# Optimization experiments

Measured on AMD Instinct MI355X. Metric: run time of the kernel, lower is better.

Reference implementation:

```python
import jax, jax.numpy as jnp
import numpy as np

HEAD_SIZE = 64
EMB_SIZE = 1024
B, N = 4, 4096


def setup_inputs() -> dict:
    key = jax.random.key(0)
    kx, kk, kq, kv = jax.random.split(key, 4)
    x = jax.random.normal(kx, (B, N, EMB_SIZE), dtype=jnp.float32)
    # nn.Linear(emb, head, bias=False): weight [head, emb]; y = x @ W.T
    s = 1.0 / np.sqrt(EMB_SIZE)
    Wk = jax.random.uniform(kk, (HEAD_SIZE, EMB_SIZE), jnp.float32, -s, s)
    Wq = jax.random.uniform(kq, (HEAD_SIZE, EMB_SIZE), jnp.float32, -s, s)
    Wv = jax.random.uniform(kv, (HEAD_SIZE, EMB_SIZE), jnp.float32, -s, s)
    return {"x": x, "Wk": Wk, "Wq": Wq, "Wv": Wv}


def reference(x, Wk, Wq, Wv):
    # k, q, v: [B, N, H]
    k = jnp.einsum("bne,he->bnh", x, Wk)
    q = jnp.einsum("bne,he->bnh", x, Wq)
    v = jnp.einsum("bne,he->bnh", x, Wv)
    scale = HEAD_SIZE ** -0.5
    aff = jnp.einsum("bqh,bkh->bqk", q, k) * scale  # [B, N, N]
    aff = jax.nn.softmax(aff, axis=2)
    # dropout rate is 0.0 -> identity
    return jnp.einsum("bqk,bkh->bqh", aff, v)
```

## Files before the change

### kernel.cpp

```cpp
#include <hip/hip_runtime.h>

#define NB   4
#define SEQ  4096
#define EMB  1024
#define HS   64

typedef __attribute__((ext_vector_type(8))) short bf16x8;
typedef __attribute__((ext_vector_type(4))) float f32x4;

__device__ inline unsigned short f2bf(float f) {
  unsigned int u = __float_as_uint(f);
  u += 0x7fffu + ((u >> 16) & 1u);
  return (unsigned short)(u >> 16);
}
__device__ inline float bf2f(unsigned short h) {
  return __uint_as_float(((unsigned int)h) << 16);
}
__device__ inline int swzi64(int row, int c) {
  return row * 64 + ((c ^ (row & 7)) << 3);
}
__device__ inline int swzi32(int row, int c) {
  return row * 32 + ((c ^ ((row >> 1) & 3)) << 3);
}
__device__ inline int swzi128(int row, int c) {
  return row * 128 + ((c ^ (row & 7)) << 3);
}
__device__ inline void gld16(const unsigned short* g, unsigned short* l) {
  __builtin_amdgcn_global_load_lds(
      (const __attribute__((address_space(1))) void*)g,
      (__attribute__((address_space(3))) void*)l, 16, 0, 0);
}

__global__ __launch_bounds__(256) void wprep(
    const float* __restrict__ Wk, const float* __restrict__ Wq,
    const float* __restrict__ Wv,
    unsigned short* __restrict__ Wh, unsigned short* __restrict__ Wl) {
  int i = blockIdx.x * 256 + threadIdx.x;
  int e = i >> 8, c = i & 255;
  float4 v;
  float sc = 1.0f;
  if (e < 64)       { v = ((const float4*)Wq)[e * 256 + c];
                      sc = 0.18033688011112042f; }
  else if (e < 128)   v = ((const float4*)Wk)[(e - 64) * 256 + c];
  else                v = ((const float4*)Wv)[(e - 128) * 256 + c];
  v.x *= sc; v.y *= sc; v.z *= sc; v.w *= sc;
  ushort4 hv, lv;
  hv.x = f2bf(v.x); lv.x = f2bf(v.x - bf2f(hv.x));
  hv.y = f2bf(v.y); lv.y = f2bf(v.y - bf2f(hv.y));
  hv.z = f2bf(v.z); lv.z = f2bf(v.z - bf2f(hv.z));
  hv.w = f2bf(v.w); lv.w = f2bf(v.w - bf2f(hv.w));
  *(ushort4*)&Wh[i * 4] = hv;
  *(ushort4*)&Wl[i * 4] = lv;
}

#define XhSp(p) ((unsigned short*)(SM + (p) * 2048))
#define XlSp(p) ((unsigned short*)(SM + 4096 + (p) * 2048))
#define WhSp(p) ((unsigned short*)(SM + 8192 + (p) * 12288))
#define WlSp(p) ((unsigned short*)(SM + 32768 + (p) * 12288))

__global__ __launch_bounds__(256) void qkv_x1(
    const float* __restrict__ x,
    const unsigned short* __restrict__ Wh, const unsigned short* __restrict__ Wl,
    unsigned short* __restrict__ qh, unsigned short* __restrict__ ql,
    unsigned short* __restrict__ kh, unsigned short* __restrict__ kl,
    unsigned short* __restrict__ vt) {
  __shared__ __align__(16) unsigned char SM[57344];

  const int t  = threadIdx.x;
  const int l  = t & 63;
  const int li = l & 15;
  const int g  = l >> 4;
  const int w  = t >> 6;
  const int m0 = blockIdx.x * 32;
  const int b  = m0 >> 12;
  const int n0 = m0 & 4095;

  const int xrow = t >> 3;
  const float* xp = x + (m0 + xrow) * EMB + (t & 7) * 4;
  const int xaddr = xrow * 32 + ((((t & 7) >> 1) ^ ((xrow >> 1) & 3)) << 3)
                    + (t & 1) * 4;

  const int wconst = (l >> 2) * EMB + (((l & 3) ^ ((l >> 3) & 3)) << 3);

  f32x4 acc[2][3];
#pragma unroll
  for (int i = 0; i < 2; ++i)
#pragma unroll
    for (int j = 0; j < 3; ++j) acc[i][j] = (f32x4){0.f, 0.f, 0.f, 0.f};

  const int rA0 = li, rA1 = 16 + li;
  const int rB0 = 48 * w + li, rB1 = rB0 + 16, rB2 = rB0 + 32;

  auto issueW = [&](int s, int p) {
    const int ko = s * 32;
#pragma unroll
    for (int i = 0; i < 3; ++i) {
      const int seg = 3 * w + i;
      gld16(Wh + 16 * seg * EMB + wconst + ko, WhSp(p) + seg * 512);
      gld16(Wl + 16 * seg * EMB + wconst + ko, WlSp(p) + seg * 512);
    }
  };
  auto writeX = [&](float4 v, int p) {
    unsigned short h0 = f2bf(v.x), h1 = f2bf(v.y), h2 = f2bf(v.z), h3 = f2bf(v.w);
    unsigned short e0 = f2bf(v.x - bf2f(h0)), e1 = f2bf(v.y - bf2f(h1));
    unsigned short e2 = f2bf(v.z - bf2f(h2)), e3 = f2bf(v.w - bf2f(h3));
    int2 hv, lv;
    hv.x = (int)((unsigned)h0 | ((unsigned)h1 << 16));
    hv.y = (int)((unsigned)h2 | ((unsigned)h3 << 16));
    lv.x = (int)((unsigned)e0 | ((unsigned)e1 << 16));
    lv.y = (int)((unsigned)e2 | ((unsigned)e3 << 16));
    *(int2*)&XhSp(p)[xaddr] = hv;
    *(int2*)&XlSp(p)[xaddr] = lv;
  };

  float4 px = *(const float4*)xp;
  issueW(0, 0);
  writeX(px, 0);
  px = *(const float4*)(xp + 32);
  __syncthreads();

  for (int s = 0; s < 32; ++s) {
    const int p = s & 1;
    if (s < 31) {
      issueW(s + 1, p ^ 1);
      writeX(px, p ^ 1);
      if (s < 30) px = *(const float4*)(xp + (s + 2) * 32);
    } else {
      asm volatile("s_waitcnt vmcnt(0)" ::: "memory");
    }
    __builtin_amdgcn_sched_barrier(0);

    bf16x8 ah0 = *(const bf16x8*)&XhSp(p)[swzi32(rA0, g)];
    bf16x8 ah1 = *(const bf16x8*)&XhSp(p)[swzi32(rA1, g)];
    bf16x8 al0 = *(const bf16x8*)&XlSp(p)[swzi32(rA0, g)];
    bf16x8 al1 = *(const bf16x8*)&XlSp(p)[swzi32(rA1, g)];
    bf16x8 bh0 = *(const bf16x8*)&WhSp(p)[swzi32(rB0, g)];
    bf16x8 bh1 = *(const bf16x8*)&WhSp(p)[swzi32(rB1, g)];
    bf16x8 bh2 = *(const bf16x8*)&WhSp(p)[swzi32(rB2, g)];
    bf16x8 bl0 = *(const bf16x8*)&WlSp(p)[swzi32(rB0, g)];
    bf16x8 bl1 = *(const bf16x8*)&WlSp(p)[swzi32(rB1, g)];
    bf16x8 bl2 = *(const bf16x8*)&WlSp(p)[swzi32(rB2, g)];

    __builtin_amdgcn_s_setprio(1);
    acc[0][0] = __builtin_amdgcn_mfma_f32_16x16x32_bf16(ah0, bh0, acc[0][0], 0,0,0);
    acc[0][0] = __builtin_amdgcn_mfma_f32_16x16x32_bf16(ah0, bl0, acc[0][0], 0,0,0);
    acc[0][0] = __builtin_amdgcn_mfma_f32_16x16x32_bf16(al0, bh0, acc[0][0], 0,0,0);
    acc[0][1] = __builtin_amdgcn_mfma_f32_16x16x32_bf16(ah0, bh1, acc[0][1], 0,0,0);
    acc[0][1] = __builtin_amdgcn_mfma_f32_16x16x32_bf16(ah0, bl1, acc[0][1], 0,0,0);
    acc[0][1] = __builtin_amdgcn_mfma_f32_16x16x32_bf16(al0, bh1, acc[0][1], 0,0,0);
    acc[0][2] = __builtin_amdgcn_mfma_f32_16x16x32_bf16(ah0, bh2, acc[0][2], 0,0,0);
    acc[0][2] = __builtin_amdgcn_mfma_f32_16x16x32_bf16(ah0, bl2, acc[0][2], 0,0,0);
    acc[0][2] = __builtin_amdgcn_mfma_f32_16x16x32_bf16(al0, bh2, acc[0][2], 0,0,0);
    acc[1][0] = __builtin_amdgcn_mfma_f32_16x16x32_bf16(ah1, bh0, acc[1][0], 0,0,0);
    acc[1][0] = __builtin_amdgcn_mfma_f32_16x16x32_bf16(ah1, bl0, acc[1][0], 0,0,0);
    acc[1][0] = __builtin_amdgcn_mfma_f32_16x16x32_bf16(al1, bh0, acc[1][0], 0,0,0);
    acc[1][1] = __builtin_amdgcn_mfma_f32_16x16x32_bf16(ah1, bh1, acc[1][1], 0,0,0);
    acc[1][1] = __builtin_amdgcn_mfma_f32_16x16x32_bf16(ah1, bl1, acc[1][1], 0,0,0);
    acc[1][1] = __builtin_amdgcn_mfma_f32_16x16x32_bf16(al1, bh1, acc[1][1], 0,0,0);
    acc[1][2] = __builtin_amdgcn_mfma_f32_16x16x32_bf16(ah1, bh2, acc[1][2], 0,0,0);
    acc[1][2] = __builtin_amdgcn_mfma_f32_16x16x32_bf16(ah1, bl2, acc[1][2], 0,0,0);
    acc[1][2] = __builtin_amdgcn_mfma_f32_16x16x32_bf16(al1, bh2, acc[1][2], 0,0,0);
    __builtin_amdgcn_s_setprio(0);

    asm volatile("s_waitcnt lgkmcnt(0)" ::: "memory");
    __builtin_amdgcn_s_barrier();
    __builtin_amdgcn_sched_barrier(0);
  }

#pragma unroll
  for (int i = 0; i < 2; ++i)
#pragma unroll
    for (int j = 0; j < 3; ++j) {
      const int H3 = 48 * w + 16 * j + li;
#pragma unroll
      for (int r = 0; r < 4; ++r) {
        const int mrow = 16 * i + 4 * g + r;
        const float vv = acc[i][j][r];
        if (H3 < 64) {
          const unsigned short hb = f2bf(vv);
          const int off = (b * SEQ + n0 + mrow) * HS + H3;
          qh[off] = hb; ql[off] = f2bf(vv - bf2f(hb));
        } else if (H3 < 128) {
          const unsigned short hb = f2bf(vv);
          const int off = (b * SEQ + n0 + mrow) * HS + (H3 - 64);
          kh[off] = hb; kl[off] = f2bf(vv - bf2f(hb));
        } else {
          vt[(b * HS + (H3 - 128)) * SEQ + n0 + mrow] = f2bf(vv);
        }
      }
    }
}

__global__ __launch_bounds__(512) void attn_mfma(
    const unsigned short* __restrict__ qh, const unsigned short* __restrict__ ql,
    const unsigned short* __restrict__ kh, const unsigned short* __restrict__ kl,
    const unsigned short* __restrict__ vt, float* __restrict__ out) {
  __shared__ __align__(16) unsigned char SM[118784];
  unsigned short* const PtS = (unsigned short*)(SM + 98304);

  const int t  = threadIdx.x;
  const int l  = t & 63;
  const int li = l & 15;
  const int g  = l >> 4;
  const int w  = t >> 6;
  const int qg = w & 1;
  const int ks = w >> 1;
  const int b  = blockIdx.y;
  const int q0 = blockIdx.x << 6;

  bf16x8 qfh[2][2], qfl[2][2];
#pragma unroll
  for (int qs = 0; qs < 2; ++qs) {
    const unsigned short* qrh = qh + (b * SEQ + q0 + 32 * qg + 16 * qs + li) * HS;
    const unsigned short* qrl = ql + (b * SEQ + q0 + 32 * qg + 16 * qs + li) * HS;
    qfh[qs][0] = *(const bf16x8*)&qrh[8 * g];
    qfh[qs][1] = *(const bf16x8*)&qrh[32 + 8 * g];
    qfl[qs][0] = *(const bf16x8*)&qrl[8 * g];
    qfl[qs][1] = *(const bf16x8*)&qrl[32 + 8 * g];
  }

  const int kconst = (l >> 3) * HS + (((l & 7) ^ (l >> 3)) << 3);
  const int rowl = l >> 4, slot = l & 15;
  const int vcE = rowl * SEQ + ((slot ^ rowl) << 3);
  const int vcO = rowl * SEQ + ((slot ^ (4 + rowl)) << 3);
  const unsigned short* khB = kh + b * SEQ * HS;
  const unsigned short* klB = kl + b * SEQ * HS;
  const unsigned short* vtB = vt + b * HS * SEQ;
  const int sA = 2 * w, sB = 2 * w + 1;

  f32x4 O[4][2];
#pragma unroll
  for (int ht = 0; ht < 4; ++ht) {
    O[ht][0] = (f32x4){0.f, 0.f, 0.f, 0.f};
    O[ht][1] = (f32x4){0.f, 0.f, 0.f, 0.f};
  }
  float lp0 = 0.f, lp1 = 0.f;
  unsigned short* const PtW = PtS + w * 1280;

  auto stage = [&](int it, int p) {
    const int kt0 = it << 7;
    unsigned short* const KhP = (unsigned short*)(SM + p * 16384);
    unsigned short* const KlP = (unsigned short*)(SM + 32768 + p * 16384);
    unsigned short* const VtP = (unsigned short*)(SM + 65536 + p * 16384);
    gld16(khB + (kt0 + 8 * sA) * HS + kconst, KhP + sA * 512);
    gld16(khB + (kt0 + 8 * sB) * HS + kconst, KhP + sB * 512);
    gld16(klB + (kt0 + 8 * sA) * HS + kconst, KlP + sA * 512);
    gld16(klB + (kt0 + 8 * sB) * HS + kconst, KlP + sB * 512);
    gld16(vtB + 4 * sA * SEQ + kt0 + vcE, VtP + sA * 512);
    gld16(vtB + 4 * sB * SEQ + kt0 + vcO, VtP + sB * 512);
  };

  stage(0, 0);
  __syncthreads();

  for (int it = 0; it < 32; ++it) {
    const int p = it & 1;
    if (it < 31) stage(it + 1, p ^ 1);

    unsigned short* const KhS = (unsigned short*)(SM + p * 16384);
    unsigned short* const KlS = (unsigned short*)(SM + 32768 + p * 16384);
    unsigned short* const VtS = (unsigned short*)(SM + 65536 + p * 16384);

    f32x4 S[2][2];
    S[0][0] = (f32x4){-32.f, -32.f, -32.f, -32.f};
    S[0][1] = (f32x4){-32.f, -32.f, -32.f, -32.f};
    S[1][0] = (f32x4){-32.f, -32.f, -32.f, -32.f};
    S[1][1] = (f32x4){-32.f, -32.f, -32.f, -32.f};
    __builtin_amdgcn_s_setprio(1);
#pragma unroll
    for (int khf = 0; khf < 2; ++khf) {
      const int cc = 4 * khf + g;
#pragma unroll
      for (int kt = 0; kt < 2; ++kt) {
        const int row = 32 * ks + 16 * kt + li;
        bf16x8 akh = *(const bf16x8*)&KhS[swzi64(row, cc)];
        bf16x8 akl = *(const bf16x8*)&KlS[swzi64(row, cc)];
        S[kt][0] = __builtin_amdgcn_mfma_f32_16x16x32_bf16(akh, qfh[0][khf], S[kt][0], 0,0,0);
        S[kt][0] = __builtin_amdgcn_mfma_f32_16x16x32_bf16(akh, qfl[0][khf], S[kt][0], 0,0,0);
        S[kt][0] = __builtin_amdgcn_mfma_f32_16x16x32_bf16(akl, qfh[0][khf], S[kt][0], 0,0,0);
        S[kt][1] = __builtin_amdgcn_mfma_f32_16x16x32_bf16(akh, qfh[1][khf], S[kt][1], 0,0,0);
        S[kt][1] = __builtin_amdgcn_mfma_f32_16x16x32_bf16(akh, qfl[1][khf], S[kt][1], 0,0,0);
        S[kt][1] = __builtin_amdgcn_mfma_f32_16x16x32_bf16(akl, qfh[1][khf], S[kt][1], 0,0,0);
      }
    }
    __builtin_amdgcn_s_setprio(0);

#pragma unroll
    for (int kt = 0; kt < 2; ++kt)
#pragma unroll
      for (int qs = 0; qs < 2; ++qs) {
        unsigned pu[4];
        float ls = 0.f;
#pragma unroll
        for (int r = 0; r < 4; ++r) {
          const float pe = exp2f(S[kt][qs][r]);
          pu[r] = __float_as_uint(pe);
          ls += __uint_as_float(pu[r] & 0xffff0000u);
        }
        if (qs == 0) lp0 += ls; else lp1 += ls;
        const unsigned p01 = __builtin_amdgcn_perm(pu[1], pu[0], 0x07060302u);
        const unsigned p23 = __builtin_amdgcn_perm(pu[3], pu[2], 0x07060302u);
        const int qrow = 16 * qs + li;
        const int c = 2 * kt + (g >> 1);
        const int addr = qrow * 40 + (((c ^ (qrow & 3))) << 3) + ((g & 1) << 2);
        int2 pv; pv.x = (int)p01; pv.y = (int)p23;
        *(int2*)&PtW[addr] = pv;
      }

    asm volatile("" ::: "memory");

    bf16x8 pb0 = *(const bf16x8*)&PtW[li * 40 + ((g ^ (li & 3)) << 3)];
    {
      const int r1 = 16 + li;
      bf16x8 pb1 = *(const bf16x8*)&PtW[r1 * 40 + ((g ^ (r1 & 3)) << 3)];
      __builtin_amdgcn_s_setprio(1);
#pragma unroll
      for (int ht = 0; ht < 4; ++ht) {
        const int vrow = 16 * ht + li;
        bf16x8 va = *(const bf16x8*)&VtS[swzi128(vrow, 4 * ks + g)];
        O[ht][0] = __builtin_amdgcn_mfma_f32_16x16x32_bf16(va, pb0, O[ht][0], 0,0,0);
        O[ht][1] = __builtin_amdgcn_mfma_f32_16x16x32_bf16(va, pb1, O[ht][1], 0,0,0);
      }
      __builtin_amdgcn_s_setprio(0);
    }

    __syncthreads();
  }


  lp0 += __shfl_xor(lp0, 16); lp0 += __shfl_xor(lp0, 32);
  lp1 += __shfl_xor(lp1, 16); lp1 += __shfl_xor(lp1, 32);

  float* const OTm = (float*)SM;
  float* const Lm  = (float*)(SM + 65536);
#pragma unroll
  for (int ht = 0; ht < 4; ++ht)
#pragma unroll
    for (int qs = 0; qs < 2; ++qs) {
      float4 o4;
      o4.x = O[ht][qs][0]; o4.y = O[ht][qs][1];
      o4.z = O[ht][qs][2]; o4.w = O[ht][qs][3];
      *(float4*)&OTm[w * 2048 + (16 * qs + li) * 64 + 16 * ht + 4 * g] = o4;
    }
  if (g == 0) { Lm[w * 32 + li] = lp0; Lm[w * 32 + 16 + li] = lp1; }
  __syncthreads();

  {
    const int q = t >> 3, h8 = (t & 7) << 3;
    const int qq = q & 31, qgf = q >> 5;
    float lF = 0.f;
    float4 a = {0.f, 0.f, 0.f, 0.f}, c4 = {0.f, 0.f, 0.f, 0.f};
#pragma unroll
    for (int k2 = 0; k2 < 4; ++k2) {
      const int ww = qgf + 2 * k2;
      lF += Lm[ww * 32 + qq];
      const float* Ob = OTm + ww * 2048 + qq * 64 + h8;
      float4 u = *(const float4*)Ob;
      float4 v = *(const float4*)(Ob + 4);
      a.x += u.x; a.y += u.y; a.z += u.z; a.w += u.w;
      c4.x += v.x; c4.y += v.y; c4.z += v.z; c4.w += v.w;
    }
    const float inv = 1.f / lF;
    a.x *= inv; a.y *= inv; a.z *= inv; a.w *= inv;
    c4.x *= inv; c4.y *= inv; c4.z *= inv; c4.w *= inv;
    float* op = out + (b * SEQ + q0 + q) * HS + h8;
    *(float4*)op = a;
    *(float4*)(op + 4) = c4;
  }
}

extern "C" void kernel_launch(void* const* d_in, const int* in_sizes, int n_in,
                              void* d_out, int out_size, void* d_ws,
                              size_t ws_size, hipStream_t stream) {
  const float* x  = (const float*)d_in[0];
  const float* Wk = (const float*)d_in[1];
  const float* Wq = (const float*)d_in[2];
  const float* Wv = (const float*)d_in[3];
  float* out = (float*)d_out;

  unsigned short* us = (unsigned short*)d_ws;
  unsigned short* qh = us + 0 * (1 << 20);
  unsigned short* ql = us + 1 * (1 << 20);
  unsigned short* kh = us + 2 * (1 << 20);
  unsigned short* kl = us + 3 * (1 << 20);
  unsigned short* vt = us + 4 * (1 << 20);
  unsigned short* Wh = us + 5 * (1 << 20);
  unsigned short* Wl = Wh + 192 * 1024;

  wprep<<<192, 256, 0, stream>>>(Wk, Wq, Wv, Wh, Wl);
  qkv_x1<<<512, 256, 0, stream>>>(x, Wh, Wl, qh, ql, kh, kl, vt);
  attn_mfma<<<dim3(64, NB), 512, 0, stream>>>(qh, ql, kh, kl, vt, out);
}
```

Baseline: 186.8 us.

## Load QKV weight fragments directly into registers instead of staging through LDS

The QKV projection kernel now reads the bf16 hi/lo weight fragments straight from global memory into double-buffered registers, dropping the 48KB LDS staging buffers for weights. Shared memory falls to 8KB, and launch bounds request two blocks per CU to raise occupancy. The x prefetch is deepened to two steps ahead, and the LDS write is moved after the MFMAs. The risk is that each wave re-reads weights from L2/global with less coalesced 16-byte loads, and register pressure rises.

```diff
diff --git a/kernel.cpp b/kernel.cpp
--- a/kernel.cpp
+++ b/kernel.cpp
@@ -55,16 +55,14 @@
 
 #define XhSp(p) ((unsigned short*)(SM + (p) * 2048))
 #define XlSp(p) ((unsigned short*)(SM + 4096 + (p) * 2048))
-#define WhSp(p) ((unsigned short*)(SM + 8192 + (p) * 12288))
-#define WlSp(p) ((unsigned short*)(SM + 32768 + (p) * 12288))
-
-__global__ __launch_bounds__(256) void qkv_x1(
+
+__global__ __launch_bounds__(256, 2) void qkv_x1(
     const float* __restrict__ x,
     const unsigned short* __restrict__ Wh, const unsigned short* __restrict__ Wl,
     unsigned short* __restrict__ qh, unsigned short* __restrict__ ql,
     unsigned short* __restrict__ kh, unsigned short* __restrict__ kl,
     unsigned short* __restrict__ vt) {
-  __shared__ __align__(16) unsigned char SM[57344];
+  __shared__ __align__(16) unsigned char SM[8192];
 
   const int t  = threadIdx.x;
   const int l  = t & 63;
@@ -80,7 +78,13 @@
   const int xaddr = xrow * 32 + ((((t & 7) >> 1) ^ ((xrow >> 1) & 3)) << 3)
                     + (t & 1) * 4;
 
-  const int wconst = (l >> 2) * EMB + (((l & 3) ^ ((l >> 3) & 3)) << 3);
+  const int r0 = 48 * w + li, r1 = r0 + 16, r2 = r0 + 32;
+  const unsigned short* const Wh0 = Wh + r0 * EMB + 8 * g;
+  const unsigned short* const Wh1 = Wh + r1 * EMB + 8 * g;
+  const unsigned short* const Wh2 = Wh + r2 * EMB + 8 * g;
+  const unsigned short* const Wl0 = Wl + r0 * EMB + 8 * g;
+  const unsigned short* const Wl1 = Wl + r1 * EMB + 8 * g;
+  const unsigned short* const Wl2 = Wl + r2 * EMB + 8 * g;
 
   f32x4 acc[2][3];
 #pragma unroll
@@ -89,16 +93,15 @@
     for (int j = 0; j < 3; ++j) acc[i][j] = (f32x4){0.f, 0.f, 0.f, 0.f};
 
   const int rA0 = li, rA1 = 16 + li;
-  const int rB0 = 48 * w + li, rB1 = rB0 + 16, rB2 = rB0 + 32;
-
-  auto issueW = [&](int s, int p) {
+
+  auto loadB = [&](int s, bf16x8 (&B)[6]) {
     const int ko = s * 32;
-#pragma unroll
-    for (int i = 0; i < 3; ++i) {
-      const int seg = 3 * w + i;
-      gld16(Wh + 16 * seg * EMB + wconst + ko, WhSp(p) + seg * 512);
-      gld16(Wl + 16 * seg * EMB + wconst + ko, WlSp(p) + seg * 512);
-    }
+    B[0] = *(const bf16x8*)&Wh0[ko];
+    B[1] = *(const bf16x8*)&Wh1[ko];
+    B[2] = *(const bf16x8*)&Wh2[ko];
+    B[3] = *(const bf16x8*)&Wl0[ko];
+    B[4] = *(const bf16x8*)&Wl1[ko];
+    B[5] = *(const bf16x8*)&Wl2[ko];
   };
   auto writeX = [&](float4 v, int p) {
     unsigned short h0 = f2bf(v.x), h1 = f2bf(v.y), h2 = f2bf(v.z), h3 = f2bf(v.w);
@@ -113,58 +116,57 @@
     *(int2*)&XlSp(p)[xaddr] = lv;
   };
 
-  float4 px = *(const float4*)xp;
-  issueW(0, 0);
-  writeX(px, 0);
-  px = *(const float4*)(xp + 32);
+  bf16x8 B0[6], B1[6];
+  loadB(0, B0);
+  writeX(*(const float4*)xp, 0);
+  float4 pxA = *(const float4*)(xp + 32);
+  float4 pxB = *(const float4*)(xp + 64);
   __syncthreads();
 
-  for (int s = 0; s < 32; ++s) {
+  auto step = [&](int s, bf16x8 (&Bc)[6], bf16x8 (&Bn)[6]) {
     const int p = s & 1;
-    if (s < 31) {
-      issueW(s + 1, p ^ 1);
-      writeX(px, p ^ 1);
-      if (s < 30) px = *(const float4*)(xp + (s + 2) * 32);
-    } else {
-      asm volatile("s_waitcnt vmcnt(0)" ::: "memory");
-    }
-    __builtin_amdgcn_sched_barrier(0);
+    if (s < 31) loadB(s + 1, Bn);
 
     bf16x8 ah0 = *(const bf16x8*)&XhSp(p)[swzi32(rA0, g)];
     bf16x8 ah1 = *(const bf16x8*)&XhSp(p)[swzi32(rA1, g)];
     bf16x8 al0 = *(const bf16x8*)&XlSp(p)[swzi32(rA0, g)];
     bf16x8 al1 = *(const bf16x8*)&XlSp(p)[swzi32(rA1, g)];
-    bf16x8 bh0 = *(const bf16x8*)&WhSp(p)[swzi32(rB0, g)];
-    bf16x8 bh1 = *(const bf16x8*)&WhSp(p)[swzi32(rB1, g)];
-    bf16x8 bh2 = *(const bf16x8*)&WhSp(p)[swzi32(rB2, g)];
-    bf16x8 bl0 = *(const bf16x8*)&WlSp(p)[swzi32(rB0, g)];
-    bf16x8 bl1 = *(const bf16x8*)&WlSp(p)[swzi32(rB1, g)];
-    bf16x8 bl2 = *(const bf16x8*)&WlSp(p)[swzi32(rB2, g)];
 
     __builtin_amdgcn_s_setprio(1);
-    acc[0][0] = __builtin_amdgcn_mfma_f32_16x16x32_bf16(ah0, bh0, acc[0][0], 0,0,0);
-    acc[0][0] = __builtin_amdgcn_mfma_f32_16x16x32_bf16(ah0, bl0, acc[0][0], 0,0,0);
-    acc[0][0] = __builtin_amdgcn_mfma_f32_16x16x32_bf16(al0, bh0, acc[0][0], 0,0,0);
-    acc[0][1] = __builtin_amdgcn_mfma_f32_16x16x32_bf16(ah0, bh1, acc[0][1], 0,0,0);
-    acc[0][1] = __builtin_amdgcn_mfma_f32_16x16x32_bf16(ah0, bl1, acc[0][1], 0,0,0);
-    acc[0][1] = __builtin_amdgcn_mfma_f32_16x16x32_bf16(al0, bh1, acc[0][1], 0,0,0);
-    acc[0][2] = __builtin_amdgcn_mfma_f32_16x16x32_bf16(ah0, bh2, acc[0][2], 0,0,0);
-    acc[0][2] = __builtin_amdgcn_mfma_f32_16x16x32_bf16(ah0, bl2, acc[0][2], 0,0,0);
-    acc[0][2] = __builtin_amdgcn_mfma_f32_16x16x32_bf16(al0, bh2, acc[0][2], 0,0,0);
-    acc[1][0] = __builtin_amdgcn_mfma_f32_16x16x32_bf16(ah1, bh0, acc[1][0], 0,0,0);
-    acc[1][0] = __builtin_amdgcn_mfma_f32_16x16x32_bf16(ah1, bl0, acc[1][0], 0,0,0);
-    acc[1][0] = __builtin_amdgcn_mfma_f32_16x16x32_bf16(al1, bh0, acc[1][0], 0,0,0);
-    acc[1][1] = __builtin_amdgcn_mfma_f32_16x16x32_bf16(ah1, bh1, acc[1][1], 0,0,0);
-    acc[1][1] = __builtin_amdgcn_mfma_f32_16x16x32_bf16(ah1, bl1, acc[1][1], 0,0,0);
-    acc[1][1] = __builtin_amdgcn_mfma_f32_16x16x32_bf16(al1, bh1, acc[1][1], 0,0,0);
-    acc[1][2] = __builtin_amdgcn_mfma_f32_16x16x32_bf16(ah1, bh2, acc[1][2], 0,0,0);
-    acc[1][2] = __builtin_amdgcn_mfma_f32_16x16x32_bf16(ah1, bl2, acc[1][2], 0,0,0);
-    acc[1][2] = __builtin_amdgcn_mfma_f32_16x16x32_bf16(al1, bh2, acc[1][2], 0,0,0);
+    acc[0][0] = __builtin_amdgcn_mfma_f32_16x16x32_bf16(ah0, Bc[0], acc[0][0], 0,0,0);
+    acc[0][0] = __builtin_amdgcn_mfma_f32_16x16x32_bf16(ah0, Bc[3], acc[0][0], 0,0,0);
+    acc[0][0] = __builtin_amdgcn_mfma_f32_16x16x32_bf16(al0, Bc[0], acc[0][0], 0,0,0);
+    acc[0][1] = __builtin_amdgcn_mfma_f32_16x16x32_bf16(ah0, Bc[1], acc[0][1], 0,0,0);
+    acc[0][1] = __builtin_amdgcn_mfma_f32_16x16x32_bf16(ah0, Bc[4], acc[0][1], 0,0,0);
+    acc[0][1] = __builtin_amdgcn_mfma_f32_16x16x32_bf16(al0, Bc[1], acc[0][1], 0,0,0);
+    acc[0][2] = __builtin_amdgcn_mfma_f32_16x16x32_bf16(ah0, Bc[2], acc[0][2], 0,0,0);
+    acc[0][2] = __builtin_amdgcn_mfma_f32_16x16x32_bf16(ah0, Bc[5], acc[0][2], 0,0,0);
+    acc[0][2] = __builtin_amdgcn_mfma_f32_16x16x32_bf16(al0, Bc[2], acc[0][2], 0,0,0);
+    acc[1][0] = __builtin_amdgcn_mfma_f32_16x16x32_bf16(ah1, Bc[0], acc[1][0], 0,0,0);
+    acc[1][0] = __builtin_amdgcn_mfma_f32_16x16x32_bf16(ah1, Bc[3], acc[1][0], 0,0,0);
+    acc[1][0] = __builtin_amdgcn_mfma_f32_16x16x32_bf16(al1, Bc[0], acc[1][0], 0,0,0);
+    acc[1][1] = __builtin_amdgcn_mfma_f32_16x16x32_bf16(ah1, Bc[1], acc[1][1], 0,0,0);
+    acc[1][1] = __builtin_amdgcn_mfma_f32_16x16x32_bf16(ah1, Bc[4], acc[1][1], 0,0,0);
+    acc[1][1] = __builtin_amdgcn_mfma_f32_16x16x32_bf16(al1, Bc[1], acc[1][1], 0,0,0);
+    acc[1][2] = __builtin_amdgcn_mfma_f32_16x16x32_bf16(ah1, Bc[2], acc[1][2], 0,0,0);
+    acc[1][2] = __builtin_amdgcn_mfma_f32_16x16x32_bf16(ah1, Bc[5], acc[1][2], 0,0,0);
+    acc[1][2] = __builtin_amdgcn_mfma_f32_16x16x32_bf16(al1, Bc[2], acc[1][2], 0,0,0);
     __builtin_amdgcn_s_setprio(0);
+
+    if (s < 31) {
+      writeX(pxA, p ^ 1);
+      pxA = pxB;
+      if (s < 29) pxB = *(const float4*)(xp + (s + 3) * 32);
+    }
 
     asm volatile("s_waitcnt lgkmcnt(0)" ::: "memory");
     __builtin_amdgcn_s_barrier();
     __builtin_amdgcn_sched_barrier(0);
+  };
+
+  for (int s2 = 0; s2 < 16; ++s2) {
+    step(2 * s2,     B0, B1);
+    step(2 * s2 + 1, B1, B0);
   }
 
 #pragma unroll
```

Measured after the change: 197.8 us. +5.9%, slower.

## Software-pipeline PV matmul one iteration behind QK and exp

Applied to the files above, without the earlier changes.

Splits each attention iteration so the P·V MFMA for the previous key tile runs right after the current QK^T MFMAs, while the exp/pack of the current tile follows. V gets a triple-buffered LDS slot and P gets a double-buffered per-wave slab, which raises shared memory from about 116KB to 152KB. The aim is to interleave the exp work with the matrix-core work and to drop the in-iteration dependency between writing P and reading it back. The cost is more LDS, an extra epilogue PV call, and added register pressure.

```diff
diff --git a/kernel.cpp b/kernel.cpp
--- a/kernel.cpp
+++ b/kernel.cpp
@@ -195,8 +195,8 @@
     const unsigned short* __restrict__ qh, const unsigned short* __restrict__ ql,
     const unsigned short* __restrict__ kh, const unsigned short* __restrict__ kl,
     const unsigned short* __restrict__ vt, float* __restrict__ out) {
-  __shared__ __align__(16) unsigned char SM[118784];
-  unsigned short* const PtS = (unsigned short*)(SM + 98304);
+  __shared__ __align__(16) unsigned char SM[155648];
+  unsigned short* const PtS = (unsigned short*)(SM + 114688);
 
   const int t  = threadIdx.x;
   const int l  = t & 63;
@@ -235,13 +235,12 @@
     O[ht][1] = (f32x4){0.f, 0.f, 0.f, 0.f};
   }
   float lp0 = 0.f, lp1 = 0.f;
-  unsigned short* const PtW = PtS + w * 1280;
-
-  auto stage = [&](int it, int p) {
+
+  auto stage = [&](int it, int pK, int vb) {
     const int kt0 = it << 7;
-    unsigned short* const KhP = (unsigned short*)(SM + p * 16384);
-    unsigned short* const KlP = (unsigned short*)(SM + 32768 + p * 16384);
-    unsigned short* const VtP = (unsigned short*)(SM + 65536 + p * 16384);
+    unsigned short* const KhP = (unsigned short*)(SM + pK * 16384);
+    unsigned short* const KlP = (unsigned short*)(SM + 32768 + pK * 16384);
+    unsigned short* const VtP = (unsigned short*)(SM + 65536 + vb * 16384);
     gld16(khB + (kt0 + 8 * sA) * HS + kconst, KhP + sA * 512);
     gld16(khB + (kt0 + 8 * sB) * HS + kconst, KhP + sB * 512);
     gld16(klB + (kt0 + 8 * sA) * HS + kconst, KlP + sA * 512);
@@ -250,16 +249,34 @@
     gld16(vtB + 4 * sB * SEQ + kt0 + vcO, VtP + sB * 512);
   };
 
-  stage(0, 0);
+  auto PV = [&](int slab, int vb) {
+    unsigned short* const PtP = PtS + w * 2560 + slab * 1280;
+    unsigned short* const VtP = (unsigned short*)(SM + 65536 + vb * 16384);
+    bf16x8 pb0 = *(const bf16x8*)&PtP[li * 40 + ((g ^ (li & 3)) << 3)];
+    const int r1 = 16 + li;
+    bf16x8 pb1 = *(const bf16x8*)&PtP[r1 * 40 + ((g ^ (r1 & 3)) << 3)];
+    __builtin_amdgcn_s_setprio(1);
+#pragma unroll
+    for (int ht = 0; ht < 4; ++ht) {
+      const int vrow = 16 * ht + li;
+      bf16x8 va = *(const bf16x8*)&VtP[swzi128(vrow, 4 * ks + g)];
+      O[ht][0] = __builtin_amdgcn_mfma_f32_16x16x32_bf16(va, pb0, O[ht][0], 0,0,0);
+      O[ht][1] = __builtin_amdgcn_mfma_f32_16x16x32_bf16(va, pb1, O[ht][1], 0,0,0);
+    }
+    __builtin_amdgcn_s_setprio(0);
+  };
+
+  stage(0, 0, 0);
   __syncthreads();
 
+  int vbn = 1;
+  int vbp = 2;
   for (int it = 0; it < 32; ++it) {
     const int p = it & 1;
-    if (it < 31) stage(it + 1, p ^ 1);
+    if (it < 31) stage(it + 1, p ^ 1, vbn);
 
     unsigned short* const KhS = (unsigned short*)(SM + p * 16384);
     unsigned short* const KlS = (unsigned short*)(SM + 32768 + p * 16384);
-    unsigned short* const VtS = (unsigned short*)(SM + 65536 + p * 16384);
 
     f32x4 S[2][2];
     S[0][0] = (f32x4){-32.f, -32.f, -32.f, -32.f};
@@ -285,6 +302,9 @@
     }
     __builtin_amdgcn_s_setprio(0);
 
+    if (it > 0) PV(p ^ 1, vbp);
+
+    unsigned short* const PtW = PtS + w * 2560 + p * 1280;
 #pragma unroll
     for (int kt = 0; kt < 2; ++kt)
 #pragma unroll
@@ -307,26 +327,13 @@
         *(int2*)&PtW[addr] = pv;
       }
 
-    asm volatile("" ::: "memory");
-
-    bf16x8 pb0 = *(const bf16x8*)&PtW[li * 40 + ((g ^ (li & 3)) << 3)];
-    {
-      const int r1 = 16 + li;
-      bf16x8 pb1 = *(const bf16x8*)&PtW[r1 * 40 + ((g ^ (r1 & 3)) << 3)];
-      __builtin_amdgcn_s_setprio(1);
-#pragma unroll
-      for (int ht = 0; ht < 4; ++ht) {
-        const int vrow = 16 * ht + li;
-        bf16x8 va = *(const bf16x8*)&VtS[swzi128(vrow, 4 * ks + g)];
-        O[ht][0] = __builtin_amdgcn_mfma_f32_16x16x32_bf16(va, pb0, O[ht][0], 0,0,0);
-        O[ht][1] = __builtin_amdgcn_mfma_f32_16x16x32_bf16(va, pb1, O[ht][1], 0,0,0);
-      }
-      __builtin_amdgcn_s_setprio(0);
-    }
-
     __syncthreads();
+
+    vbn = (vbn == 2) ? 0 : vbn + 1;
+    vbp = (vbp == 2) ? 0 : vbp + 1;
   }
 
+  PV(1, 1);
 
   lp0 += __shfl_xor(lp0, 16); lp0 += __shfl_xor(lp0, 32);
   lp1 += __shfl_xor(lp1, 16); lp1 += __shfl_xor(lp1, 32);
```

New measurement: 183.8 us. Within noise of the previous version (-1.6%).
